# Kernel tuning notes

Hardware: AMD Instinct MI355X
Metric: run time of the kernel (lower is better)

## Reference

```python
import jax, jax.numpy as jnp
import numpy as np

B = 65536
IN = 256
H = 256
COMB = IN + H


def setup_inputs() -> dict:
    key = jax.random.key(0)
    ks = jax.random.split(key, 11)
    s_in = 1.0 / np.sqrt(COMB)
    inp = {
        "x_t": jax.random.normal(ks[0], (B, IN), dtype=jnp.float32),
        "h_prev": jax.random.normal(ks[1], (B, H), dtype=jnp.float32),
        "c_prev": jax.random.normal(ks[2], (B, H), dtype=jnp.float32),
        # nn.Linear weights: [out, in] layout, uniform(-1/sqrt(in), 1/sqrt(in))
        "W_f": jax.random.uniform(ks[3], (H, COMB), jnp.float32, -s_in, s_in),
        "b_f": jax.random.uniform(ks[4], (H,), jnp.float32, -s_in, s_in),
        "W_i": jax.random.uniform(ks[5], (H, COMB), jnp.float32, -s_in, s_in),
        "b_i": jax.random.uniform(ks[6], (H,), jnp.float32, -s_in, s_in),
        "W_o": jax.random.uniform(ks[7], (H, COMB), jnp.float32, -s_in, s_in),
        "b_o": jax.random.uniform(ks[8], (H,), jnp.float32, -s_in, s_in),
        "W_g": jax.random.uniform(ks[9], (H, COMB), jnp.float32, -s_in, s_in),
        "b_g": jax.random.uniform(ks[10], (H,), jnp.float32, -s_in, s_in),
    }
    return inp


def reference(x_t, h_prev, c_prev, W_f, b_f, W_i, b_i, W_o, b_o, W_g, b_g):
    combined = jnp.concatenate([x_t, h_prev], axis=-1)  # [B, COMB]
    # Stack the four gate weights into one GEMM: [B, COMB] @ [COMB, 4H]
    W = jnp.concatenate([W_f, W_i, W_o, W_g], axis=0)   # [4H, COMB]
    b = jnp.concatenate([b_f, b_i, b_o, b_g], axis=0)   # [4H]
    gates = combined @ W.T + b                           # [B, 4H]
    f_lin, i_lin, o_lin, g_lin = jnp.split(gates, 4, axis=-1)
    f_t = jax.nn.sigmoid(f_lin)
    i_t = jax.nn.sigmoid(i_lin)
    o_t = jax.nn.sigmoid(o_lin)
    g_t = jnp.tanh(g_lin)
    c_t = f_t * c_prev + i_t * g_t
    h_t = o_t * jnp.tanh(c_t)
    return (h_t, c_t, f_t, i_t, o_t, g_t)
```

## Files before the change

kernel.cpp:

```cpp
#include <hip/hip_runtime.h>
#include <cstdint>
#include <cstddef>

#define B_SZ 65536
#define K_SZ 512

typedef __attribute__((ext_vector_type(8))) short bf16x8;
typedef __attribute__((ext_vector_type(8))) unsigned short u16x8;
typedef __attribute__((ext_vector_type(4))) float f32x4;

__device__ __forceinline__ unsigned short f2bf(float f) {
  union { float f; uint32_t u; } v; v.f = f;
  uint32_t u = v.u;
  uint32_t r = (u + 0x7FFFu + ((u >> 16) & 1u)) >> 16;
  return (unsigned short)r;
}

__global__ __launch_bounds__(256) void pack_a_kernel(const float* __restrict__ x,
                                                     const float* __restrict__ hp,
                                                     unsigned short* __restrict__ out) {
  int i = blockIdx.x * 256 + threadIdx.x;
  int row = i >> 6, c = i & 63;
  const float* src = (c < 32) ? (x + ((size_t)row << 8) + ((size_t)c << 3))
                              : (hp + ((size_t)row << 8) + ((size_t)(c - 32) << 3));
  float4 v0 = ((const float4*)src)[0];
  float4 v1 = ((const float4*)src)[1];
  u16x8 o;
  o[0] = f2bf(v0.x); o[1] = f2bf(v0.y); o[2] = f2bf(v0.z); o[3] = f2bf(v0.w);
  o[4] = f2bf(v1.x); o[5] = f2bf(v1.y); o[6] = f2bf(v1.z); o[7] = f2bf(v1.w);
  *((u16x8*)(out + ((size_t)i << 3))) = o;
}

__global__ __launch_bounds__(256) void pack_w_kernel(const float* __restrict__ Wf,
                                                     const float* __restrict__ Wi,
                                                     const float* __restrict__ Wo,
                                                     const float* __restrict__ Wg,
                                                     unsigned short* __restrict__ out) {
  int i = blockIdx.x * 256 + threadIdx.x;
  int rho = i >> 6, c = i & 63;
  int bn = rho >> 7, r = rho & 127;
  int hhblk = (r >> 6) & 1, gate = (r >> 4) & 3, hh = r & 15;
  int srow = bn * 32 + hhblk * 16 + hh;
  const float* W = (gate == 0) ? Wf : (gate == 1) ? Wi : (gate == 2) ? Wo : Wg;
  const float* src = W + (size_t)srow * 512 + ((size_t)c << 3);
  float4 v0 = ((const float4*)src)[0];
  float4 v1 = ((const float4*)src)[1];
  u16x8 o;
  o[0] = f2bf(v0.x); o[1] = f2bf(v0.y); o[2] = f2bf(v0.z); o[3] = f2bf(v0.w);
  o[4] = f2bf(v1.x); o[5] = f2bf(v1.y); o[6] = f2bf(v1.z); o[7] = f2bf(v1.w);
  *((u16x8*)(out + ((size_t)i << 3))) = o;
}

__device__ __forceinline__ float sigmoid_f(float x) {
  return __builtin_amdgcn_rcpf(1.f + __expf(-x));
}
__device__ __forceinline__ float tanh_f(float x) {
  return 1.f - 2.f * __builtin_amdgcn_rcpf(__expf(2.f * x) + 1.f);
}

__global__ __launch_bounds__(256, 2) void lstm_gemm_kernel(
    const unsigned short* __restrict__ A, const unsigned short* __restrict__ Wb,
    const float* __restrict__ c_prev,
    const float* __restrict__ bf_, const float* __restrict__ bi_,
    const float* __restrict__ bo_, const float* __restrict__ bg_,
    float* __restrict__ out) {
  __shared__ __align__(16) unsigned short As[128 * 64];
  __shared__ __align__(16) unsigned short Bs[128 * 64];
  const int bn = blockIdx.x;
  const int m0 = blockIdx.y << 7;
  const int t = threadIdx.x;
  const int lane = t & 63, w = t >> 6;
  const int r15 = lane & 15, quad = lane >> 4;

  f32x4 zero = {0.f, 0.f, 0.f, 0.f};
  f32x4 acc[4][4];
#pragma unroll
  for (int a = 0; a < 4; ++a)
#pragma unroll
    for (int b = 0; b < 4; ++b) acc[a][b] = zero;

  const int mbase = (w & 1) << 6;
  const int nbase = (w >> 1) << 6;

  for (int kt = 0; kt < 8; ++kt) {
    const int k0 = kt << 6;
    if (kt) __syncthreads();
#pragma unroll
    for (int j = 0; j < 4; ++j) {
      int l = (j << 8) + t;
      int row = l >> 3, st = l & 7;
      int c = st ^ (row & 7);
      const unsigned short* ga = A + (size_t)(m0 + row) * 512 + k0 + (c << 3);
      __builtin_amdgcn_global_load_lds(
          (const __attribute__((address_space(1))) void*)ga,
          (__attribute__((address_space(3))) void*)(As + ((size_t)l << 3)), 16, 0, 0);
      const unsigned short* gb = Wb + (size_t)((bn << 7) + row) * 512 + k0 + (c << 3);
      __builtin_amdgcn_global_load_lds(
          (const __attribute__((address_space(1))) void*)gb,
          (__attribute__((address_space(3))) void*)(Bs + ((size_t)l << 3)), 16, 0, 0);
    }
    __syncthreads();
#pragma unroll
    for (int ks = 0; ks < 2; ++ks) {
      bf16x8 af[4], bfr[4];
      const int ch = (ks << 2) + quad;
#pragma unroll
      for (int mi = 0; mi < 4; ++mi) {
        int row = mbase + (mi << 4) + r15;
        af[mi] = *((const bf16x8*)(As + (row << 6) + ((ch ^ (row & 7)) << 3)));
      }
#pragma unroll
      for (int gi = 0; gi < 4; ++gi) {
        int row = nbase + (gi << 4) + r15;
        bfr[gi] = *((const bf16x8*)(Bs + (row << 6) + ((ch ^ (row & 7)) << 3)));
      }
#pragma unroll
      for (int mi = 0; mi < 4; ++mi)
#pragma unroll
        for (int gi = 0; gi < 4; ++gi)
          acc[mi][gi] = __builtin_amdgcn_mfma_f32_16x16x32_bf16(af[mi], bfr[gi],
                                                                acc[mi][gi], 0, 0, 0);
    }
  }

  const int h = (bn << 5) + ((w >> 1) << 4) + r15;
  const float Bf = bf_[h], Bi = bi_[h], Bo = bo_[h], Bg = bg_[h];
  const size_t S = (size_t)B_SZ * 256;
#pragma unroll
  for (int mi = 0; mi < 4; ++mi) {
    const int mr0 = m0 + mbase + (mi << 4) + (quad << 2);
#pragma unroll
    for (int r = 0; r < 4; ++r) {
      const int m = mr0 + r;
      float F = acc[mi][0][r] + Bf;
      float I = acc[mi][1][r] + Bi;
      float O = acc[mi][2][r] + Bo;
      float G = acc[mi][3][r] + Bg;
      float f = sigmoid_f(F);
      float ii = sigmoid_f(I);
      float o = sigmoid_f(O);
      float g = tanh_f(G);
      size_t base = (size_t)m * 256 + h;
      float cp = c_prev[base];
      float ct = f * cp + ii * g;
      float ht = o * tanh_f(ct);
      out[base] = ht;
      out[S + base] = ct;
      out[2 * S + base] = f;
      out[3 * S + base] = ii;
      out[4 * S + base] = o;
      out[5 * S + base] = g;
    }
  }
}

extern "C" void kernel_launch(void* const* d_in, const int* in_sizes, int n_in,
                              void* d_out, int out_size, void* d_ws, size_t ws_size,
                              hipStream_t stream) {
  const float* x   = (const float*)d_in[0];
  const float* hp  = (const float*)d_in[1];
  const float* cp  = (const float*)d_in[2];
  const float* Wf  = (const float*)d_in[3];
  const float* bf_ = (const float*)d_in[4];
  const float* Wi  = (const float*)d_in[5];
  const float* bi_ = (const float*)d_in[6];
  const float* Wo  = (const float*)d_in[7];
  const float* bo_ = (const float*)d_in[8];
  const float* Wg  = (const float*)d_in[9];
  const float* bg_ = (const float*)d_in[10];
  float* out = (float*)d_out;

  unsigned short* Apack = (unsigned short*)d_ws;
  unsigned short* Wb = (unsigned short*)((char*)d_ws + (size_t)B_SZ * 512 * 2);

  pack_a_kernel<<<dim3((B_SZ * 64) / 256), dim3(256), 0, stream>>>(x, hp, Apack);
  pack_w_kernel<<<dim3((1024 * 64) / 256), dim3(256), 0, stream>>>(Wf, Wi, Wo, Wg, Wb);
  lstm_gemm_kernel<<<dim3(8, 512), dim3(256), 0, stream>>>(Apack, Wb, cp, bf_, bi_,
                                                           bo_, bg_, out);
}
```

Baseline: 640.8 us.

## Fuse activation bf16 packing into GEMM with double-buffered LDS and larger N tile

Removes the separate pack kernel for x/h_prev: the fused kernel loads fp32 activations into registers, converts them to bf16 and writes them into LDS. The loop is double-buffered, so the next tile's loads overlap the current MFMA work. The block grows to 512 threads with a 128x256 output tile, and an XCD-aware block-to-tile mapping is added. This removes an extra write and read of the bf16 A matrix through global memory, at the cost of more LDS, more registers and conversion work inside the GEMM loop.

```diff
diff --git a/kernel.cpp b/kernel.cpp
--- a/kernel.cpp
+++ b/kernel.cpp
@@ -3,7 +3,6 @@
 #include <cstddef>
 
 #define B_SZ 65536
-#define K_SZ 512
 
 typedef __attribute__((ext_vector_type(8))) short bf16x8;
 typedef __attribute__((ext_vector_type(8))) unsigned short u16x8;
@@ -14,21 +13,6 @@
   uint32_t u = v.u;
   uint32_t r = (u + 0x7FFFu + ((u >> 16) & 1u)) >> 16;
   return (unsigned short)r;
-}
-
-__global__ __launch_bounds__(256) void pack_a_kernel(const float* __restrict__ x,
-                                                     const float* __restrict__ hp,
-                                                     unsigned short* __restrict__ out) {
-  int i = blockIdx.x * 256 + threadIdx.x;
-  int row = i >> 6, c = i & 63;
-  const float* src = (c < 32) ? (x + ((size_t)row << 8) + ((size_t)c << 3))
-                              : (hp + ((size_t)row << 8) + ((size_t)(c - 32) << 3));
-  float4 v0 = ((const float4*)src)[0];
-  float4 v1 = ((const float4*)src)[1];
-  u16x8 o;
-  o[0] = f2bf(v0.x); o[1] = f2bf(v0.y); o[2] = f2bf(v0.z); o[3] = f2bf(v0.w);
-  o[4] = f2bf(v1.x); o[5] = f2bf(v1.y); o[6] = f2bf(v1.z); o[7] = f2bf(v1.w);
-  *((u16x8*)(out + ((size_t)i << 3))) = o;
 }
 
 __global__ __launch_bounds__(256) void pack_w_kernel(const float* __restrict__ Wf,
@@ -38,9 +22,10 @@
                                                      unsigned short* __restrict__ out) {
   int i = blockIdx.x * 256 + threadIdx.x;
   int rho = i >> 6, c = i & 63;
-  int bn = rho >> 7, r = rho & 127;
-  int hhblk = (r >> 6) & 1, gate = (r >> 4) & 3, hh = r & 15;
-  int srow = bn * 32 + hhblk * 16 + hh;
+  int bn = rho >> 8;
+  int r = rho & 255;
+  int wc = r >> 6, gate = (r >> 4) & 3, hh = r & 15;
+  int srow = (bn << 6) + (wc << 4) + hh;
   const float* W = (gate == 0) ? Wf : (gate == 1) ? Wi : (gate == 2) ? Wo : Wg;
   const float* src = W + (size_t)srow * 512 + ((size_t)c << 3);
   float4 v0 = ((const float4*)src)[0];
@@ -58,19 +43,33 @@
   return 1.f - 2.f * __builtin_amdgcn_rcpf(__expf(2.f * x) + 1.f);
 }
 
-__global__ __launch_bounds__(256, 2) void lstm_gemm_kernel(
-    const unsigned short* __restrict__ A, const unsigned short* __restrict__ Wb,
-    const float* __restrict__ c_prev,
+__global__ __launch_bounds__(512, 2) void lstm_fused_kernel(
+    const float* __restrict__ X, const float* __restrict__ Hp,
+    const unsigned short* __restrict__ Wb, const float* __restrict__ c_prev,
     const float* __restrict__ bf_, const float* __restrict__ bi_,
     const float* __restrict__ bo_, const float* __restrict__ bg_,
     float* __restrict__ out) {
-  __shared__ __align__(16) unsigned short As[128 * 64];
-  __shared__ __align__(16) unsigned short Bs[128 * 64];
-  const int bn = blockIdx.x;
-  const int m0 = blockIdx.y << 7;
+  __shared__ __align__(16) unsigned short As[2][128 * 64];
+  __shared__ __align__(16) unsigned short Bs[2][256 * 64];
+
+  const int L = blockIdx.x;
+  const int xcd = L & 7, slot = L >> 3;
+  const int mt = (xcd << 6) + (slot >> 2);
+  const int bn = slot & 3;
+  const int m0 = mt << 7;
+
   const int t = threadIdx.x;
   const int lane = t & 63, w = t >> 6;
   const int r15 = lane & 15, quad = lane >> 4;
+  const int mbase = (w >> 2) << 6;
+  const int nbase = (w & 3) << 6;
+
+  const int h = (bn << 6) + ((w & 3) << 4) + r15;
+  const float Bf = bf_[h], Bi = bi_[h], Bo = bo_[h], Bg = bg_[h];
+
+  const int la0 = t, la1 = t + 512;
+  const int ar0 = la0 >> 3, ar1 = la1 >> 3;
+  const int ac0 = (la0 & 7) ^ (ar0 & 7), ac1 = (la1 & 7) ^ (ar1 & 7);
 
   f32x4 zero = {0.f, 0.f, 0.f, 0.f};
   f32x4 acc[4][4];
@@ -79,27 +78,45 @@
 #pragma unroll
     for (int b = 0; b < 4; ++b) acc[a][b] = zero;
 
-  const int mbase = (w & 1) << 6;
-  const int nbase = (w >> 1) << 6;
-
-  for (int kt = 0; kt < 8; ++kt) {
+  float4 av[4];
+
+  auto load_A = [&](int kt) {
+    const float* src = (kt < 4) ? X : Hp;
+    const int kcol = (kt & 3) << 6;
+    const float* p0 = src + (size_t)(m0 + ar0) * 256 + kcol + (ac0 << 3);
+    const float* p1 = src + (size_t)(m0 + ar1) * 256 + kcol + (ac1 << 3);
+    av[0] = ((const float4*)p0)[0];
+    av[1] = ((const float4*)p0)[1];
+    av[2] = ((const float4*)p1)[0];
+    av[3] = ((const float4*)p1)[1];
+  };
+
+  auto write_A = [&](int buf) {
+    u16x8 o0, o1;
+    o0[0] = f2bf(av[0].x); o0[1] = f2bf(av[0].y); o0[2] = f2bf(av[0].z); o0[3] = f2bf(av[0].w);
+    o0[4] = f2bf(av[1].x); o0[5] = f2bf(av[1].y); o0[6] = f2bf(av[1].z); o0[7] = f2bf(av[1].w);
+    o1[0] = f2bf(av[2].x); o1[1] = f2bf(av[2].y); o1[2] = f2bf(av[2].z); o1[3] = f2bf(av[2].w);
+    o1[4] = f2bf(av[3].x); o1[5] = f2bf(av[3].y); o1[6] = f2bf(av[3].z); o1[7] = f2bf(av[3].w);
+    *((u16x8*)&As[buf][la0 << 3]) = o0;
+    *((u16x8*)&As[buf][la1 << 3]) = o1;
+  };
+
+  auto stage_B = [&](int buf, int kt) {
     const int k0 = kt << 6;
-    if (kt) __syncthreads();
-#pragma unroll
-    for (int j = 0; j < 4; ++j) {
-      int l = (j << 8) + t;
+#pragma unroll
+    for (int jj = 0; jj < 4; ++jj) {
+      int l = (jj << 9) + t;
       int row = l >> 3, st = l & 7;
       int c = st ^ (row & 7);
-      const unsigned short* ga = A + (size_t)(m0 + row) * 512 + k0 + (c << 3);
-      __builtin_amdgcn_global_load_lds(
-          (const __attribute__((address_space(1))) void*)ga,
-          (__attribute__((address_space(3))) void*)(As + ((size_t)l << 3)), 16, 0, 0);
-      const unsigned short* gb = Wb + (size_t)((bn << 7) + row) * 512 + k0 + (c << 3);
+      const unsigned short* gb =
+          Wb + (size_t)((bn << 8) + row) * 512 + k0 + (c << 3);
       __builtin_amdgcn_global_load_lds(
           (const __attribute__((address_space(1))) void*)gb,
-          (__attribute__((address_space(3))) void*)(Bs + ((size_t)l << 3)), 16, 0, 0);
-    }
-    __syncthreads();
+          (__attribute__((address_space(3))) void*)(&Bs[buf][l << 3]), 16, 0, 0);
+    }
+  };
+
+  auto compute = [&](int buf) {
 #pragma unroll
     for (int ks = 0; ks < 2; ++ks) {
       bf16x8 af[4], bfr[4];
@@ -107,24 +124,39 @@
 #pragma unroll
       for (int mi = 0; mi < 4; ++mi) {
         int row = mbase + (mi << 4) + r15;
-        af[mi] = *((const bf16x8*)(As + (row << 6) + ((ch ^ (row & 7)) << 3)));
+        af[mi] = *((const bf16x8*)&As[buf][(row << 6) + ((ch ^ (row & 7)) << 3)]);
       }
 #pragma unroll
       for (int gi = 0; gi < 4; ++gi) {
         int row = nbase + (gi << 4) + r15;
-        bfr[gi] = *((const bf16x8*)(Bs + (row << 6) + ((ch ^ (row & 7)) << 3)));
+        bfr[gi] = *((const bf16x8*)&Bs[buf][(row << 6) + ((ch ^ (row & 7)) << 3)]);
       }
 #pragma unroll
       for (int mi = 0; mi < 4; ++mi)
 #pragma unroll
         for (int gi = 0; gi < 4; ++gi)
-          acc[mi][gi] = __builtin_amdgcn_mfma_f32_16x16x32_bf16(af[mi], bfr[gi],
-                                                                acc[mi][gi], 0, 0, 0);
-    }
+          acc[mi][gi] = __builtin_amdgcn_mfma_f32_16x16x32_bf16(
+              af[mi], bfr[gi], acc[mi][gi], 0, 0, 0);
+    }
+  };
+
+  load_A(0);
+  stage_B(0, 0);
+  write_A(0);
+  __syncthreads();
+
+#pragma unroll
+  for (int kt = 0; kt < 8; ++kt) {
+    const int cur = kt & 1, nxt = cur ^ 1;
+    if (kt < 7) {
+      load_A(kt + 1);
+      stage_B(nxt, kt + 1);
+    }
+    compute(cur);
+    if (kt < 7) write_A(nxt);
+    __syncthreads();
   }
 
-  const int h = (bn << 5) + ((w >> 1) << 4) + r15;
-  const float Bf = bf_[h], Bi = bi_[h], Bo = bo_[h], Bg = bg_[h];
   const size_t S = (size_t)B_SZ * 256;
 #pragma unroll
   for (int mi = 0; mi < 4; ++mi) {
@@ -170,11 +202,9 @@
   const float* bg_ = (const float*)d_in[10];
   float* out = (float*)d_out;
 
-  unsigned short* Apack = (unsigned short*)d_ws;
-  unsigned short* Wb = (unsigned short*)((char*)d_ws + (size_t)B_SZ * 512 * 2);
-
-  pack_a_kernel<<<dim3((B_SZ * 64) / 256), dim3(256), 0, stream>>>(x, hp, Apack);
-  pack_w_kernel<<<dim3((1024 * 64) / 256), dim3(256), 0, stream>>>(Wf, Wi, Wo, Wg, Wb);
-  lstm_gemm_kernel<<<dim3(8, 512), dim3(256), 0, stream>>>(Apack, Wb, cp, bf_, bi_,
-                                                           bo_, bg_, out);
-}
+  unsigned short* Wb = (unsigned short*)d_ws;
+
+  pack_w_kernel<<<dim3(256), dim3(256), 0, stream>>>(Wf, Wi, Wo, Wg, Wb);
+  lstm_fused_kernel<<<dim3(2048), dim3(512), 0, stream>>>(x, hp, Wb, cp, bf_, bi_,
+                                                          bo_, bg_, out);
+}
```

After: 640.2 us. About the same (-0.1%).
